# Performance work log

Hardware: AMD Instinct MI355X
Metric: run time of the kernel (lower is better)

The kernel has to match this reference:

```python
import jax, jax.numpy as jnp
import numpy as np

EMBED_DIM = 2048
N_HEADS = 16
N_KV_HEADS = 4
HEAD_DIM = EMBED_DIM // N_HEADS  # 128
B, T = 8, 512


def _rope_tables(seq, dim):
    # matches RoPE.__init__: freqs repeated twice along last dim
    inv_freq = 1.0 / (10000.0 ** (jnp.arange(0, dim, 2, dtype=jnp.float32) / dim))
    t = jnp.arange(seq, dtype=jnp.float32)
    freqs = jnp.outer(t, inv_freq)          # [T, dim/2]
    emb = jnp.concatenate([freqs, freqs], axis=-1)  # [T, dim]
    return jnp.cos(emb), jnp.sin(emb)


def _apply_rope(x, cos, sin):
    # x: [B, H, T, D]; rotate-half convention
    d2 = x.shape[-1] // 2
    x1, x2 = x[..., :d2], x[..., d2:]
    x_rot = jnp.concatenate([-x2, x1], axis=-1)
    return x * cos[None, None] + x_rot * sin[None, None]


def setup_inputs() -> dict:
    key = jax.random.key(0)
    k1, k2, k3, k4, k5 = jax.random.split(key, 5)
    x = jax.random.normal(k1, (B, T, EMBED_DIM), dtype=jnp.float32)
    s = 1.0 / np.sqrt(EMBED_DIM)
    # weights stored [in, out] for y = x @ W
    wq = jax.random.normal(k2, (EMBED_DIM, EMBED_DIM), dtype=jnp.float32) * s
    wk = jax.random.normal(k3, (EMBED_DIM, HEAD_DIM * N_KV_HEADS), dtype=jnp.float32) * s
    wv = jax.random.normal(k4, (EMBED_DIM, HEAD_DIM * N_KV_HEADS), dtype=jnp.float32) * s
    wo = jax.random.normal(k5, (EMBED_DIM, EMBED_DIM), dtype=jnp.float32) * s
    # causal mask: 1 where attendable, 0 -> masked to -inf
    mask = jnp.tril(jnp.ones((T, T), dtype=bool))[None, None]  # [1,1,T,T]
    return {"x": x, "wq": wq, "wk": wk, "wv": wv, "wo": wo, "mask": mask}


def reference(x, wq, wk, wv, wo, mask):
    Bx, Tx, C = x.shape
    rep = N_HEADS // N_KV_HEADS
    q = (x @ wq).reshape(Bx, Tx, N_HEADS, HEAD_DIM).transpose(0, 2, 1, 3)      # [B,H,T,D]
    k = (x @ wk).reshape(Bx, Tx, N_KV_HEADS, HEAD_DIM).transpose(0, 2, 1, 3)   # [B,Hk,T,D]
    v = (x @ wv).reshape(Bx, Tx, N_KV_HEADS, HEAD_DIM).transpose(0, 2, 1, 3)
    cos, sin = _rope_tables(Tx, HEAD_DIM)
    q = _apply_rope(q, cos, sin)
    k = _apply_rope(k, cos, sin)
    k = jnp.repeat(k, rep, axis=1)  # GQA expand -> [B,H,T,D]
    v = jnp.repeat(v, rep, axis=1)
    scale = HEAD_DIM ** -0.5
    attn = jnp.einsum('bhtd,bhsd->bhts', q, k) * scale  # [B,H,T,T]
    attn = jnp.where(mask, attn, -jnp.inf)
    attn = jax.nn.softmax(attn, axis=-1)
    out = jnp.einsum('bhts,bhsd->bhtd', attn, v)        # [B,H,T,D]
    out = out.transpose(0, 2, 1, 3).reshape(Bx, Tx, C)
    return out @ wo
```

## Files before the change

kernel.cpp:

```cpp
#include <hip/hip_runtime.h>
#include <hip/hip_bf16.h>
#include <stdint.h>


typedef __bf16 bf16x8 __attribute__((ext_vector_type(8)));
typedef float  f32x4  __attribute__((ext_vector_type(4)));
typedef float  f4     __attribute__((ext_vector_type(4)));
typedef unsigned short u16x8 __attribute__((ext_vector_type(8)));
typedef unsigned short u16x4 __attribute__((ext_vector_type(4)));
typedef unsigned short us;

template<int V> struct Ic { static constexpr int v = V; };

__device__ __forceinline__ float bf2f(us u) {
  unsigned int x = ((unsigned int)u) << 16;
  return __builtin_bit_cast(float, x);
}
__device__ __forceinline__ us f2bf(float f) {
  unsigned int x = __builtin_bit_cast(unsigned int, f);
  unsigned int r = x + 0x7fffu + ((x >> 16) & 1u);
  return (us)(r >> 16);
}

__device__ __forceinline__ void gload16(const void* gsrc, void* ldst) {
  auto g = (const __attribute__((address_space(1))) void*)gsrc;
  auto l = (__attribute__((address_space(3))) void*)ldst;
  __builtin_amdgcn_global_load_lds(g, l, 16, 0, 0);
}

#define BAR() __builtin_amdgcn_s_barrier()
#define LGK0() do { asm volatile("s_waitcnt lgkmcnt(0)" ::: "memory"); \
                    __builtin_amdgcn_sched_barrier(0); } while (0)

template<int N> __device__ __forceinline__ void VMW() {
  if constexpr (N == 0)      asm volatile("s_waitcnt vmcnt(0)" ::: "memory");
  else if constexpr (N == 2) asm volatile("s_waitcnt vmcnt(2)" ::: "memory");
  else if constexpr (N == 3) asm volatile("s_waitcnt vmcnt(3)" ::: "memory");
  else if constexpr (N == 4) asm volatile("s_waitcnt vmcnt(4)" ::: "memory");
  else static_assert(N == 0 || N == 2 || N == 3 || N == 4, "unsupported vmcnt");
  __builtin_amdgcn_sched_barrier(0);
}


__global__ void convx_kernel(const float* __restrict__ x, us* __restrict__ xb) {
  size_t idx = (size_t)blockIdx.x * 256 + threadIdx.x;
  const f4* p = (const f4*)(x + idx * 8);
  f4 a = p[0], b = p[1];
  u16x8 o;
#pragma unroll
  for (int e = 0; e < 4; ++e) { o[e] = f2bf(a[e]); o[4 + e] = f2bf(b[e]); }
  *(u16x8*)(xb + idx * 8) = o;
}

__global__ __launch_bounds__(256) void wtrans_all_kernel(
    const float* __restrict__ wq, const float* __restrict__ wk,
    const float* __restrict__ wv, const float* __restrict__ wo,
    us* __restrict__ wcat, us* __restrict__ wot) {
  __shared__ float lds[64][65];
  int bx = blockIdx.x;
  const float* src; us* dst; int N, rowOff, nb;
  if (bx < 32)      { src = wq; dst = wcat; N = 2048; rowOff = 0;    nb = bx; }
  else if (bx < 40) { src = wk; dst = wcat; N = 512;  rowOff = 2048; nb = bx - 32; }
  else if (bx < 48) { src = wv; dst = wcat; N = 512;  rowOff = 2560; nb = bx - 40; }
  else              { src = wo; dst = wot;  N = 2048; rowOff = 0;    nb = bx - 48; }
  const int n0 = nb * 64, k0 = blockIdx.y * 64;
  const int c = threadIdx.x & 63, rq = threadIdx.x >> 6;
#pragma unroll
  for (int i = 0; i < 16; ++i) {
    int r = i * 4 + rq;
    lds[r][c] = src[(size_t)(k0 + r) * N + n0 + c];
  }
  __syncthreads();
#pragma unroll
  for (int i = 0; i < 16; ++i) {
    int nr = i * 4 + rq;
    dst[(size_t)(rowOff + n0 + nr) * 2048 + k0 + c] = f2bf(lds[c][nr]);
  }
}

__global__ void tables_kernel(float* __restrict__ ct, float* __restrict__ st) {
  int idx = blockIdx.x * 256 + threadIdx.x;
  int i = idx & 63, t = idx >> 6;
  float inv = exp2f(-(float)i * (13.287712379549449f / 64.0f));
  float ang = (float)t * inv;
  ct[idx] = cosf(ang);
  st[idx] = sinf(ang);
}

__global__ void rope_kernel(us* __restrict__ Qh, us* __restrict__ Kh,
                            const float* __restrict__ ct, const float* __restrict__ st) {
  int idx = blockIdx.x * 256 + threadIdx.x;
  int dq = idx & 15;
  int t = (idx >> 4) & 511;
  int slot = idx >> 13;
  bool isQ = slot < 128;
  us* rowp = isQ ? (Qh + ((size_t)slot * 512 + t) * 128)
                 : (Kh + ((size_t)(slot - 128) * 512 + t) * 128);
  int d0 = dq * 4;
  u16x4 x1 = *(const u16x4*)(rowp + d0);
  u16x4 x2 = *(const u16x4*)(rowp + 64 + d0);
  f4 c = *(const f4*)(ct + t * 64 + d0);
  f4 s = *(const f4*)(st + t * 64 + d0);
  float scale = isQ ? 0.08838834764831845f : 1.0f;
  u16x4 o1, o2;
#pragma unroll
  for (int e = 0; e < 4; ++e) {
    float a = bf2f(x1[e]), b = bf2f(x2[e]);
    o1[e] = f2bf((a * c[e] - b * s[e]) * scale);
    o2[e] = f2bf((b * c[e] + a * s[e]) * scale);
  }
  *(u16x4*)(rowp + d0) = o1;
  *(u16x4*)(rowp + 64 + d0) = o2;
}

__global__ __launch_bounds__(256) void vtrans_kernel(const us* __restrict__ Vh,
                                                     us* __restrict__ Vt) {
  __shared__ us lds[64][66];
  const int bid = blockIdx.x;
  const int bhk = bid >> 4;
  const int rem = bid & 15;
  const int tt = rem >> 1, dt = rem & 1;
  const us* src = Vh + (size_t)bhk * 512 * 128;
  us* dst = Vt + (size_t)bhk * 128 * 512;
  const int c = threadIdx.x & 63, rq = threadIdx.x >> 6;
#pragma unroll
  for (int i = 0; i < 16; ++i) {
    int r = i * 4 + rq;
    lds[r][c] = src[(size_t)(tt * 64 + r) * 128 + dt * 64 + c];
  }
  __syncthreads();
#pragma unroll
  for (int i = 0; i < 16; ++i) {
    int dr = i * 4 + rq;
    dst[(size_t)(dt * 64 + dr) * 512 + tt * 64 + c] = lds[c][dr];
  }
}

template<int BM, int BN, int WM, int WN>
__device__ __forceinline__ void gemm8_core(const us* __restrict__ A,
    const us* __restrict__ Bt, const int K, const int m0, const int n0,
    us* sm, f32x4 (&acc)[BM / (16 * WM)][BN / (16 * WN)]) {
  constexpr int MF = BM / (16 * WM), NF = BN / (16 * WN);
  constexpr int MH = MF / 2, NH = NF / 2;
  constexpr int QM = MH * 16, QN = NH * 16;
  constexpr int AHALF = (BM / 2) * 64, ABUF = BM * 64, ALDS = 2 * ABUF;
  constexpr int BHALF = (BN / 2) * 64, BBUF = BN * 64;
  constexpr int AL = BM / 128, BL = BN / 128;
  const int tid = threadIdx.x, lane = tid & 63, wid = tid >> 6;
  const int wm = wid / WN, wn = wid % WN;
  const int lr = lane & 15, lq = lane >> 4;

  const f32x4 zz = {0.f, 0.f, 0.f, 0.f};
#pragma unroll
  for (int i = 0; i < MF; ++i)
#pragma unroll
    for (int j = 0; j < NF; ++j) acc[i][j] = zz;

  bf16x8 afr[MH][2], bfr[NH][2];

  auto stageA = [&](int kt, int qd, int h) {
#pragma unroll
    for (int i = 0; i < AL; ++i) {
      int c = i * 512 + tid;
      int lrow = c >> 3;
      int grow = (lrow / QM) * (2 * QM) + h * QM + (lrow % QM);
      int kcs = (c & 7) ^ (lrow & 7);
      gload16(A + (size_t)(m0 + grow) * K + (kt << 6) + (kcs << 3),
              sm + qd * ABUF + h * AHALF + c * 8);
    }
  };
  auto stageB = [&](int kt, int qd, int h) {
#pragma unroll
    for (int i = 0; i < BL; ++i) {
      int c = i * 512 + tid;
      int lrow = c >> 3;
      int grow = (lrow / QN) * (2 * QN) + h * QN + (lrow % QN);
      int kcs = (c & 7) ^ (lrow & 7);
      gload16(Bt + (size_t)(n0 + grow) * K + (kt << 6) + (kcs << 3),
              sm + ALDS + qd * BBUF + h * BHALF + c * 8);
    }
  };
  auto lda = [&](int q, int h) {
#pragma unroll
    for (int f = 0; f < MH; ++f) {
      int R = wm * QM + f * 16 + lr;
      const char* base = (const char*)(sm + q * ABUF + h * AHALF + R * 64);
      int sw = (R & 7) << 4;
#pragma unroll
      for (int ks = 0; ks < 2; ++ks)
        afr[f][ks] = *(const bf16x8*)(base + ((ks * 64 + lq * 16) ^ sw));
    }
  };
  auto ldb = [&](int q, int h) {
#pragma unroll
    for (int g = 0; g < NH; ++g) {
      int R = wn * QN + g * 16 + lr;
      const char* base = (const char*)(sm + ALDS + q * BBUF + h * BHALF + R * 64);
      int sw = (R & 7) << 4;
#pragma unroll
      for (int ks = 0; ks < 2; ++ks)
        bfr[g][ks] = *(const bf16x8*)(base + ((ks * 64 + lq * 16) ^ sw));
    }
  };
  auto mmac = [&](auto MQ, auto NQ) {
    constexpr int mq = decltype(MQ)::v, nq = decltype(NQ)::v;
    __builtin_amdgcn_s_setprio(1);
#pragma unroll
    for (int ks = 0; ks < 2; ++ks)
#pragma unroll
      for (int f = 0; f < MH; ++f)
#pragma unroll
        for (int g = 0; g < NH; ++g)
          acc[mq * MH + f][nq * NH + g] = __builtin_amdgcn_mfma_f32_16x16x32_bf16(
              afr[f][ks], bfr[g][ks], acc[mq * MH + f][nq * NH + g], 0, 0, 0);
    __builtin_amdgcn_s_setprio(0);
  };

  stageA(0, 0, 0); stageB(0, 0, 0); stageB(0, 0, 1); stageA(0, 0, 1);
  VMW<AL + BL>(); BAR();

  const int NT = K >> 6;
  for (int kt = 0; kt < NT; ++kt) {
    const int q = kt & 1, qn = q ^ 1;
    const bool pf = (kt + 1 < NT);
    lda(q, 0); ldb(q, 0);
    if (pf) stageA(kt + 1, qn, 0);
    BAR(); LGK0(); mmac(Ic<0>{}, Ic<0>{});
    if (pf) VMW<2 * AL>(); else VMW<AL>();
    BAR();
    ldb(q, 1);
    if (pf) stageB(kt + 1, qn, 0);
    BAR(); LGK0(); mmac(Ic<0>{}, Ic<1>{});
    if (pf) VMW<AL + BL>(); else VMW<0>();
    BAR();
    lda(q, 1);
    if (pf) stageB(kt + 1, qn, 1);
    BAR(); LGK0(); mmac(Ic<1>{}, Ic<1>{});
    BAR();
    ldb(q, 0);
    if (pf) stageA(kt + 1, qn, 1);
    BAR(); LGK0(); mmac(Ic<1>{}, Ic<0>{});
    if (pf) VMW<AL + BL>();
    BAR();
  }
}

__global__ __launch_bounds__(512, 2) void gemm_qkv8_kernel(const us* __restrict__ xb,
    const us* __restrict__ wcat, us* __restrict__ Qh, us* __restrict__ Kh,
    us* __restrict__ Vh) {
  __shared__ __align__(16) us sm[65536];
  const int bid = blockIdx.x;
  const int swz = (bid & 7) * 24 + (bid >> 3);
  const int m0 = (swz & 15) << 8, n0 = (swz >> 4) << 8;
  f32x4 acc[8][4];
  gemm8_core<256, 256, 2, 4>(xb, wcat, 2048, m0, n0, sm, acc);

  const int tid = threadIdx.x, lane = tid & 63, wid = tid >> 6;
  const int wm = wid >> 2, wn = wid & 3, lr = lane & 15, lq = lane >> 4;
#pragma unroll
  for (int f = 0; f < 8; ++f)
#pragma unroll
    for (int g = 0; g < 4; ++g) {
      int col = n0 + wn * 64 + g * 16 + lr;
#pragma unroll
      for (int r = 0; r < 4; ++r) {
        int row = m0 + wm * 128 + f * 16 + lq * 4 + r;
        int bb = row >> 9, t = row & 511;
        us val = f2bf(acc[f][g][r]);
        if (col < 2048) {
          Qh[((size_t)(bb * 16 + (col >> 7)) * 512 + t) * 128 + (col & 127)] = val;
        } else if (col < 2560) {
          int cc = col - 2048;
          Kh[((size_t)(bb * 4 + (cc >> 7)) * 512 + t) * 128 + (cc & 127)] = val;
        } else {
          int cc = col - 2560;
          Vh[((size_t)(bb * 4 + (cc >> 7)) * 512 + t) * 128 + (cc & 127)] = val;
        }
      }
    }
}

__global__ __launch_bounds__(512, 2) void gemm_out8_kernel(const us* __restrict__ Ob,
    const us* __restrict__ wot, float* __restrict__ out) {
  __shared__ __align__(16) us sm[49152];
  const int bid = blockIdx.x;
  const int swz = (bid & 7) * 32 + (bid >> 3);
  const int m0 = (swz & 15) << 8, n0 = (swz >> 4) << 7;
  f32x4 acc[8][2];
  gemm8_core<256, 128, 2, 4>(Ob, wot, 2048, m0, n0, sm, acc);

  const int tid = threadIdx.x, lane = tid & 63, wid = tid >> 6;
  const int wm = wid >> 2, wn = wid & 3, lr = lane & 15, lq = lane >> 4;
#pragma unroll
  for (int f = 0; f < 8; ++f)
#pragma unroll
    for (int g = 0; g < 2; ++g) {
      int col = n0 + wn * 32 + g * 16 + lr;
#pragma unroll
      for (int r = 0; r < 4; ++r) {
        int row = m0 + wm * 128 + f * 16 + lq * 4 + r;
        out[(size_t)row * 2048 + col] = acc[f][g][r];
      }
    }
}

__global__ __launch_bounds__(256) void attn_kernel(const us* __restrict__ Qh,
    const us* __restrict__ Kh, const us* __restrict__ Vt, us* __restrict__ Oh) {
  __shared__ __align__(16) us Ktile[64 * 128];
  __shared__ __align__(16) us Vtile[128 * 64];
  __shared__ __align__(16) us Plds[4 * 16 * 72];
  const int tid = threadIdx.x, lane = tid & 63, w = tid >> 6;
  const int lr = lane & 15, lq = lane >> 4;
  const int qb = blockIdx.x, bh = blockIdx.y;
  const int b = bh >> 4, h = bh & 15, kvh = h >> 2;
  const us* Kbh = Kh + (size_t)(b * 4 + kvh) * 512 * 128;
  const us* Vbh = Vt + (size_t)(b * 4 + kvh) * 128 * 512;

  const us* Qrow = Qh + ((size_t)bh * 512 + qb * 64 + w * 16 + lr) * 128;
  bf16x8 qf[4];
#pragma unroll
  for (int ks = 0; ks < 4; ++ks) qf[ks] = *(const bf16x8*)(Qrow + ks * 32 + (lq << 3));

  const f32x4 zz = {0.f, 0.f, 0.f, 0.f};
  f32x4 o[8];
#pragma unroll
  for (int i = 0; i < 8; ++i) o[i] = zz;
  float m[4], ll[4];
#pragma unroll
  for (int r = 0; r < 4; ++r) { m[r] = -1e30f; ll[r] = 0.f; }
  us* Pw = Plds + w * 16 * 72;

  for (int j = 0; j <= qb; ++j) {
    __syncthreads();
#pragma unroll
    for (int it = 0; it < 4; ++it) {
      int c = it * 256 + tid;
      int row = c >> 4, kc = c & 15;
      gload16(Kbh + (size_t)(j * 64 + row) * 128 + ((kc ^ (row & 7)) << 3),
              Ktile + (c << 3));
    }
#pragma unroll
    for (int it = 0; it < 4; ++it) {
      int c = it * 256 + tid;
      int row = c >> 3, tc = c & 7;
      gload16(Vbh + (size_t)row * 512 + j * 64 + ((tc ^ (row & 7)) << 3),
              Vtile + (c << 3));
    }
    __syncthreads();

    f32x4 s[4];
#pragma unroll
    for (int nb = 0; nb < 4; ++nb) s[nb] = zz;
#pragma unroll
    for (int ks = 0; ks < 4; ++ks) {
#pragma unroll
      for (int nb = 0; nb < 4; ++nb) {
        int row = nb * 16 + lr;
        bf16x8 kf = *(const bf16x8*)(Ktile + (row << 7) + (((ks * 4 + lq) ^ (row & 7)) << 3));
        s[nb] = __builtin_amdgcn_mfma_f32_16x16x32_bf16(qf[ks], kf, s[nb], 0, 0, 0);
      }
    }
    if (j == qb) {
#pragma unroll
      for (int nb = 0; nb < 4; ++nb)
#pragma unroll
        for (int r = 0; r < 4; ++r)
          if (nb * 16 + lr > w * 16 + lq * 4 + r) s[nb][r] = -1e30f;
    }

    float tm[4], alpha[4], rs[4];
#pragma unroll
    for (int r = 0; r < 4; ++r)
      tm[r] = fmaxf(fmaxf(s[0][r], s[1][r]), fmaxf(s[2][r], s[3][r]));
#pragma unroll
    for (int off = 1; off < 16; off <<= 1)
#pragma unroll
      for (int r = 0; r < 4; ++r)
        tm[r] = fmaxf(tm[r], __shfl_xor(tm[r], off, 64));
#pragma unroll
    for (int r = 0; r < 4; ++r) {
      float mn = fmaxf(m[r], tm[r]);
      alpha[r] = __expf(m[r] - mn);
      m[r] = mn;
    }
#pragma unroll
    for (int nb = 0; nb < 4; ++nb)
#pragma unroll
      for (int r = 0; r < 4; ++r)
        s[nb][r] = __expf(s[nb][r] - m[r]);
#pragma unroll
    for (int r = 0; r < 4; ++r)
      rs[r] = s[0][r] + s[1][r] + s[2][r] + s[3][r];
#pragma unroll
    for (int off = 1; off < 16; off <<= 1)
#pragma unroll
      for (int r = 0; r < 4; ++r)
        rs[r] += __shfl_xor(rs[r], off, 64);
#pragma unroll
    for (int r = 0; r < 4; ++r) ll[r] = ll[r] * alpha[r] + rs[r];
#pragma unroll
    for (int i = 0; i < 8; ++i)
#pragma unroll
      for (int r = 0; r < 4; ++r) o[i][r] *= alpha[r];

#pragma unroll
    for (int nb = 0; nb < 4; ++nb)
#pragma unroll
      for (int r = 0; r < 4; ++r)
        Pw[(lq * 4 + r) * 72 + nb * 16 + lr] = f2bf(s[nb][r]);

#pragma unroll
    for (int ks2 = 0; ks2 < 2; ++ks2) {
      bf16x8 pf = *(const bf16x8*)(Pw + lr * 72 + ks2 * 32 + (lq << 3));
#pragma unroll
      for (int nd = 0; nd < 8; ++nd) {
        int d = nd * 16 + lr;
        bf16x8 vf = *(const bf16x8*)(Vtile + (d << 6) + (((ks2 * 4 + lq) ^ (d & 7)) << 3));
        o[nd] = __builtin_amdgcn_mfma_f32_16x16x32_bf16(pf, vf, o[nd], 0, 0, 0);
      }
    }
  }

  float inv[4];
#pragma unroll
  for (int r = 0; r < 4; ++r) inv[r] = 1.0f / ll[r];
  const int rowb = b * 512 + qb * 64 + w * 16 + lq * 4;
  const int colb = h * 128 + lr;
#pragma unroll
  for (int nd = 0; nd < 8; ++nd)
#pragma unroll
    for (int r = 0; r < 4; ++r)
      Oh[(size_t)(rowb + r) * 2048 + colb + nd * 16] = f2bf(o[nd][r] * inv[r]);
}

extern "C" void kernel_launch(void* const* d_in, const int* in_sizes, int n_in,
                              void* d_out, int out_size, void* d_ws, size_t ws_size,
                              hipStream_t stream) {
  const float* x  = (const float*)d_in[0];
  const float* wq = (const float*)d_in[1];
  const float* wk = (const float*)d_in[2];
  const float* wv = (const float*)d_in[3];
  const float* wo = (const float*)d_in[4];
  float* out = (float*)d_out;
  char* ws = (char*)d_ws;

  us*    xb   = (us*)(ws);
  us*    wcat = (us*)(ws + 16777216);
  us*    wot  = (us*)(ws + 29360128);
  us*    Qh   = (us*)(ws + 37748736);
  us*    Kh   = (us*)(ws + 54525952);
  us*    Vh   = (us*)(ws + 58720256);
  us*    Vt   = (us*)(ws + 62914560);
  us*    Oh   = (us*)(ws + 67108864);
  float* ct   = (float*)(ws + 83886080);
  float* st   = (float*)(ws + 84017152);

  convx_kernel<<<4096, 256, 0, stream>>>(x, xb);
  wtrans_all_kernel<<<dim3(80, 32), 256, 0, stream>>>(wq, wk, wv, wo, wcat, wot);
  tables_kernel<<<128, 256, 0, stream>>>(ct, st);

  gemm_qkv8_kernel<<<192, 512, 0, stream>>>(xb, wcat, Qh, Kh, Vh);
  rope_kernel<<<5120, 256, 0, stream>>>(Qh, Kh, ct, st);
  vtrans_kernel<<<512, 256, 0, stream>>>(Vh, Vt);
  attn_kernel<<<dim3(8, 128), 256, 0, stream>>>(Qh, Kh, Vt, Oh);
  gemm_out8_kernel<<<256, 512, 0, stream>>>(Oh, wot, out);
}
```

Measured before the change: 175.0 us.

## Fuse prep kernels, apply Q RoPE in attention, write V transposed from QKV GEMM

Merges the x conversion, weight transposes and RoPE-table kernels into one prep launch. Replaces the pipelined 256x256 QKV GEMM with a simpler 128x128 single-buffered GEMM that writes V directly in transposed layout, which removes the separate V-transpose kernel. Q RoPE and scaling move into the attention kernel's Q load, so only K gets a standalone RoPE pass. Launch count and intermediate traffic drop, but the new GEMM has no software pipelining and scatters strided 2-byte stores for V.

```diff
diff --git a/kernel.cpp b/kernel.cpp
--- a/kernel.cpp
+++ b/kernel.cpp
@@ -41,99 +41,164 @@
   __builtin_amdgcn_sched_barrier(0);
 }
 
-
-__global__ void convx_kernel(const float* __restrict__ x, us* __restrict__ xb) {
-  size_t idx = (size_t)blockIdx.x * 256 + threadIdx.x;
-  const f4* p = (const f4*)(x + idx * 8);
-  f4 a = p[0], b = p[1];
-  u16x8 o;
-#pragma unroll
-  for (int e = 0; e < 4; ++e) { o[e] = f2bf(a[e]); o[4 + e] = f2bf(b[e]); }
-  *(u16x8*)(xb + idx * 8) = o;
-}
-
-__global__ __launch_bounds__(256) void wtrans_all_kernel(
-    const float* __restrict__ wq, const float* __restrict__ wk,
-    const float* __restrict__ wv, const float* __restrict__ wo,
-    us* __restrict__ wcat, us* __restrict__ wot) {
-  __shared__ float lds[64][65];
-  int bx = blockIdx.x;
-  const float* src; us* dst; int N, rowOff, nb;
-  if (bx < 32)      { src = wq; dst = wcat; N = 2048; rowOff = 0;    nb = bx; }
-  else if (bx < 40) { src = wk; dst = wcat; N = 512;  rowOff = 2048; nb = bx - 32; }
-  else if (bx < 48) { src = wv; dst = wcat; N = 512;  rowOff = 2560; nb = bx - 40; }
-  else              { src = wo; dst = wot;  N = 2048; rowOff = 0;    nb = bx - 48; }
-  const int n0 = nb * 64, k0 = blockIdx.y * 64;
-  const int c = threadIdx.x & 63, rq = threadIdx.x >> 6;
-#pragma unroll
-  for (int i = 0; i < 16; ++i) {
-    int r = i * 4 + rq;
-    lds[r][c] = src[(size_t)(k0 + r) * N + n0 + c];
+__global__ __launch_bounds__(256) void prep_kernel(
+    const float* __restrict__ x, const float* __restrict__ wq,
+    const float* __restrict__ wk, const float* __restrict__ wv,
+    const float* __restrict__ wo, us* __restrict__ xb,
+    us* __restrict__ wcat, us* __restrict__ wot,
+    float* __restrict__ ct, float* __restrict__ st) {
+  const int bid = blockIdx.x, tid = threadIdx.x;
+  if (bid < 4096) {
+    size_t idx = (size_t)bid * 256 + tid;
+    const f4* p = (const f4*)(x + idx * 8);
+    f4 a = p[0], b = p[1];
+    u16x8 o;
+#pragma unroll
+    for (int e = 0; e < 4; ++e) { o[e] = f2bf(a[e]); o[4 + e] = f2bf(b[e]); }
+    *(u16x8*)(xb + idx * 8) = o;
+  } else if (bid < 6656) {
+    __shared__ float lds[64][65];
+    int lb = bid - 4096;
+    int bx = lb % 80, ky = lb / 80;
+    const float* src; us* dst; int N, rowOff, nb;
+    if (bx < 32)      { src = wq; dst = wcat; N = 2048; rowOff = 0;    nb = bx; }
+    else if (bx < 40) { src = wk; dst = wcat; N = 512;  rowOff = 2048; nb = bx - 32; }
+    else if (bx < 48) { src = wv; dst = wcat; N = 512;  rowOff = 2560; nb = bx - 40; }
+    else              { src = wo; dst = wot;  N = 2048; rowOff = 0;    nb = bx - 48; }
+    const int n0 = nb * 64, k0 = ky * 64;
+    const int c = tid & 63, rq = tid >> 6;
+#pragma unroll
+    for (int i = 0; i < 16; ++i) {
+      int r = i * 4 + rq;
+      lds[r][c] = src[(size_t)(k0 + r) * N + n0 + c];
+    }
+    __syncthreads();
+#pragma unroll
+    for (int i = 0; i < 16; ++i) {
+      int nr = i * 4 + rq;
+      dst[(size_t)(rowOff + n0 + nr) * 2048 + k0 + c] = f2bf(lds[c][nr]);
+    }
+  } else {
+    int idx = (bid - 6656) * 256 + tid;
+    int i = idx & 63, t = idx >> 6;
+    float inv = exp2f(-(float)i * (13.287712379549449f / 64.0f));
+    float ang = (float)t * inv;
+    ct[idx] = cosf(ang);
+    st[idx] = sinf(ang);
   }
-  __syncthreads();
-#pragma unroll
-  for (int i = 0; i < 16; ++i) {
-    int nr = i * 4 + rq;
-    dst[(size_t)(rowOff + n0 + nr) * 2048 + k0 + c] = f2bf(lds[c][nr]);
-  }
-}
-
-__global__ void tables_kernel(float* __restrict__ ct, float* __restrict__ st) {
-  int idx = blockIdx.x * 256 + threadIdx.x;
-  int i = idx & 63, t = idx >> 6;
-  float inv = exp2f(-(float)i * (13.287712379549449f / 64.0f));
-  float ang = (float)t * inv;
-  ct[idx] = cosf(ang);
-  st[idx] = sinf(ang);
-}
-
-__global__ void rope_kernel(us* __restrict__ Qh, us* __restrict__ Kh,
-                            const float* __restrict__ ct, const float* __restrict__ st) {
+}
+
+__global__ void rope_k_kernel(us* __restrict__ Kh,
+                              const float* __restrict__ ct, const float* __restrict__ st) {
   int idx = blockIdx.x * 256 + threadIdx.x;
   int dq = idx & 15;
   int t = (idx >> 4) & 511;
   int slot = idx >> 13;
-  bool isQ = slot < 128;
-  us* rowp = isQ ? (Qh + ((size_t)slot * 512 + t) * 128)
-                 : (Kh + ((size_t)(slot - 128) * 512 + t) * 128);
+  us* rowp = Kh + ((size_t)slot * 512 + t) * 128;
   int d0 = dq * 4;
   u16x4 x1 = *(const u16x4*)(rowp + d0);
   u16x4 x2 = *(const u16x4*)(rowp + 64 + d0);
   f4 c = *(const f4*)(ct + t * 64 + d0);
   f4 s = *(const f4*)(st + t * 64 + d0);
-  float scale = isQ ? 0.08838834764831845f : 1.0f;
   u16x4 o1, o2;
 #pragma unroll
   for (int e = 0; e < 4; ++e) {
     float a = bf2f(x1[e]), b = bf2f(x2[e]);
-    o1[e] = f2bf((a * c[e] - b * s[e]) * scale);
-    o2[e] = f2bf((b * c[e] + a * s[e]) * scale);
+    o1[e] = f2bf(a * c[e] - b * s[e]);
+    o2[e] = f2bf(b * c[e] + a * s[e]);
   }
   *(u16x4*)(rowp + d0) = o1;
   *(u16x4*)(rowp + 64 + d0) = o2;
 }
 
-__global__ __launch_bounds__(256) void vtrans_kernel(const us* __restrict__ Vh,
-                                                     us* __restrict__ Vt) {
-  __shared__ us lds[64][66];
+__device__ __forceinline__ void gemm2_core(const us* __restrict__ A,
+    const us* __restrict__ Bt, const int K, const int m0, const int n0,
+    us* AT, us* BT, f32x4 (&acc)[4][4]) {
+  const int tid = threadIdx.x;
+  const int lane = tid & 63;
+  const int wid = tid >> 6;
+  const int wm = wid >> 1, wn = wid & 1;
+  const int lr = lane & 15, lq = lane >> 4;
+  const f32x4 zz = {0.f, 0.f, 0.f, 0.f};
+#pragma unroll
+  for (int i = 0; i < 4; ++i)
+#pragma unroll
+    for (int j = 0; j < 4; ++j) acc[i][j] = zz;
+
+  const int KT = K >> 6;
+  for (int kt = 0; kt < KT; ++kt) {
+    __syncthreads();
+#pragma unroll
+    for (int i = 0; i < 4; ++i) {
+      int c = i * 256 + tid;
+      int row = c >> 3, kc = (c & 7) ^ (row & 7);
+      gload16(A + (size_t)(m0 + row) * K + (kt << 6) + (kc << 3), AT + c * 8);
+    }
+#pragma unroll
+    for (int i = 0; i < 4; ++i) {
+      int c = i * 256 + tid;
+      int row = c >> 3, kc = (c & 7) ^ (row & 7);
+      gload16(Bt + (size_t)(n0 + row) * K + (kt << 6) + (kc << 3), BT + c * 8);
+    }
+    __syncthreads();
+#pragma unroll
+    for (int ks = 0; ks < 2; ++ks) {
+      bf16x8 af[4], bfm[4];
+#pragma unroll
+      for (int i = 0; i < 4; ++i) {
+        int R = wm * 64 + i * 16 + lr;
+        af[i] = *(const bf16x8*)((const char*)AT + R * 128 +
+                                 ((ks * 64 + lq * 16) ^ ((R & 7) << 4)));
+      }
+#pragma unroll
+      for (int j = 0; j < 4; ++j) {
+        int R = wn * 64 + j * 16 + lr;
+        bfm[j] = *(const bf16x8*)((const char*)BT + R * 128 +
+                                  ((ks * 64 + lq * 16) ^ ((R & 7) << 4)));
+      }
+#pragma unroll
+      for (int i = 0; i < 4; ++i)
+#pragma unroll
+        for (int j = 0; j < 4; ++j)
+          acc[i][j] = __builtin_amdgcn_mfma_f32_16x16x32_bf16(af[i], bfm[j], acc[i][j], 0, 0, 0);
+    }
+  }
+}
+
+__global__ __launch_bounds__(256, 4) void gemm_qkv2_kernel(const us* __restrict__ xb,
+    const us* __restrict__ wcat, us* __restrict__ Qh, us* __restrict__ Kh,
+    us* __restrict__ Vt) {
+  __shared__ __align__(16) us AT[128 * 64];
+  __shared__ __align__(16) us BT[128 * 64];
   const int bid = blockIdx.x;
-  const int bhk = bid >> 4;
-  const int rem = bid & 15;
-  const int tt = rem >> 1, dt = rem & 1;
-  const us* src = Vh + (size_t)bhk * 512 * 128;
-  us* dst = Vt + (size_t)bhk * 128 * 512;
-  const int c = threadIdx.x & 63, rq = threadIdx.x >> 6;
-#pragma unroll
-  for (int i = 0; i < 16; ++i) {
-    int r = i * 4 + rq;
-    lds[r][c] = src[(size_t)(tt * 64 + r) * 128 + dt * 64 + c];
-  }
-  __syncthreads();
-#pragma unroll
-  for (int i = 0; i < 16; ++i) {
-    int dr = i * 4 + rq;
-    dst[(size_t)(dt * 64 + dr) * 512 + tt * 64 + c] = lds[c][dr];
-  }
+  const int swz = (bid & 7) * 96 + (bid >> 3);
+  const int m0 = (swz & 31) << 7, n0 = (swz >> 5) << 7;
+  f32x4 acc[4][4];
+  gemm2_core(xb, wcat, 2048, m0, n0, AT, BT, acc);
+
+  const int tid = threadIdx.x, lane = tid & 63, wid = tid >> 6;
+  const int wm = wid >> 1, wn = wid & 1, lr = lane & 15, lq = lane >> 4;
+#pragma unroll
+  for (int i = 0; i < 4; ++i)
+#pragma unroll
+    for (int j = 0; j < 4; ++j) {
+      int col = n0 + wn * 64 + j * 16 + lr;
+#pragma unroll
+      for (int r = 0; r < 4; ++r) {
+        int row = m0 + wm * 64 + i * 16 + lq * 4 + r;
+        int bb = row >> 9, t = row & 511;
+        us val = f2bf(acc[i][j][r]);
+        if (col < 2048) {
+          Qh[((size_t)(bb * 16 + (col >> 7)) * 512 + t) * 128 + (col & 127)] = val;
+        } else if (col < 2560) {
+          int cc = col - 2048;
+          Kh[((size_t)(bb * 4 + (cc >> 7)) * 512 + t) * 128 + (cc & 127)] = val;
+        } else {
+          int cc = col - 2560;
+          Vt[((size_t)(bb * 4 + (cc >> 7)) * 128 + (cc & 127)) * 512 + t] = val;
+        }
+      }
+    }
 }
 
 template<int BM, int BN, int WM, int WN>
@@ -245,41 +310,6 @@
   }
 }
 
-__global__ __launch_bounds__(512, 2) void gemm_qkv8_kernel(const us* __restrict__ xb,
-    const us* __restrict__ wcat, us* __restrict__ Qh, us* __restrict__ Kh,
-    us* __restrict__ Vh) {
-  __shared__ __align__(16) us sm[65536];
-  const int bid = blockIdx.x;
-  const int swz = (bid & 7) * 24 + (bid >> 3);
-  const int m0 = (swz & 15) << 8, n0 = (swz >> 4) << 8;
-  f32x4 acc[8][4];
-  gemm8_core<256, 256, 2, 4>(xb, wcat, 2048, m0, n0, sm, acc);
-
-  const int tid = threadIdx.x, lane = tid & 63, wid = tid >> 6;
-  const int wm = wid >> 2, wn = wid & 3, lr = lane & 15, lq = lane >> 4;
-#pragma unroll
-  for (int f = 0; f < 8; ++f)
-#pragma unroll
-    for (int g = 0; g < 4; ++g) {
-      int col = n0 + wn * 64 + g * 16 + lr;
-#pragma unroll
-      for (int r = 0; r < 4; ++r) {
-        int row = m0 + wm * 128 + f * 16 + lq * 4 + r;
-        int bb = row >> 9, t = row & 511;
-        us val = f2bf(acc[f][g][r]);
-        if (col < 2048) {
-          Qh[((size_t)(bb * 16 + (col >> 7)) * 512 + t) * 128 + (col & 127)] = val;
-        } else if (col < 2560) {
-          int cc = col - 2048;
-          Kh[((size_t)(bb * 4 + (cc >> 7)) * 512 + t) * 128 + (cc & 127)] = val;
-        } else {
-          int cc = col - 2560;
-          Vh[((size_t)(bb * 4 + (cc >> 7)) * 512 + t) * 128 + (cc & 127)] = val;
-        }
-      }
-    }
-}
-
 __global__ __launch_bounds__(512, 2) void gemm_out8_kernel(const us* __restrict__ Ob,
     const us* __restrict__ wot, float* __restrict__ out) {
   __shared__ __align__(16) us sm[49152];
@@ -305,7 +335,8 @@
 }
 
 __global__ __launch_bounds__(256) void attn_kernel(const us* __restrict__ Qh,
-    const us* __restrict__ Kh, const us* __restrict__ Vt, us* __restrict__ Oh) {
+    const us* __restrict__ Kh, const us* __restrict__ Vt, us* __restrict__ Oh,
+    const float* __restrict__ ct, const float* __restrict__ st) {
   __shared__ __align__(16) us Ktile[64 * 128];
   __shared__ __align__(16) us Vtile[128 * 64];
   __shared__ __align__(16) us Plds[4 * 16 * 72];
@@ -316,10 +347,28 @@
   const us* Kbh = Kh + (size_t)(b * 4 + kvh) * 512 * 128;
   const us* Vbh = Vt + (size_t)(b * 4 + kvh) * 128 * 512;
 
-  const us* Qrow = Qh + ((size_t)bh * 512 + qb * 64 + w * 16 + lr) * 128;
+  const int t_abs = qb * 64 + w * 16 + lr;
+  const us* Qrow = Qh + ((size_t)bh * 512 + t_abs) * 128;
   bf16x8 qf[4];
-#pragma unroll
-  for (int ks = 0; ks < 4; ++ks) qf[ks] = *(const bf16x8*)(Qrow + ks * 32 + (lq << 3));
+  {
+    const float* cp = ct + t_abs * 64 + (lq << 3);
+    const float* sp = st + t_abs * 64 + (lq << 3);
+#pragma unroll
+    for (int ks = 0; ks < 2; ++ks) {
+      u16x8 a = *(const u16x8*)(Qrow + ks * 32 + (lq << 3));
+      u16x8 bb2 = *(const u16x8*)(Qrow + 64 + ks * 32 + (lq << 3));
+      u16x8 oa, ob;
+#pragma unroll
+      for (int e = 0; e < 8; ++e) {
+        float c = cp[ks * 32 + e], s = sp[ks * 32 + e];
+        float av = bf2f(a[e]), bv = bf2f(bb2[e]);
+        oa[e] = f2bf((av * c - bv * s) * 0.08838834764831845f);
+        ob[e] = f2bf((bv * c + av * s) * 0.08838834764831845f);
+      }
+      qf[ks] = __builtin_bit_cast(bf16x8, oa);
+      qf[ks + 2] = __builtin_bit_cast(bf16x8, ob);
+    }
+  }
 
   const f32x4 zz = {0.f, 0.f, 0.f, 0.f};
   f32x4 o[8];
@@ -449,19 +498,14 @@
   us*    wot  = (us*)(ws + 29360128);
   us*    Qh   = (us*)(ws + 37748736);
   us*    Kh   = (us*)(ws + 54525952);
-  us*    Vh   = (us*)(ws + 58720256);
-  us*    Vt   = (us*)(ws + 62914560);
+  us*    Vt   = (us*)(ws + 58720256);
   us*    Oh   = (us*)(ws + 67108864);
   float* ct   = (float*)(ws + 83886080);
   float* st   = (float*)(ws + 84017152);
 
-  convx_kernel<<<4096, 256, 0, stream>>>(x, xb);
-  wtrans_all_kernel<<<dim3(80, 32), 256, 0, stream>>>(wq, wk, wv, wo, wcat, wot);
-  tables_kernel<<<128, 256, 0, stream>>>(ct, st);
-
-  gemm_qkv8_kernel<<<192, 512, 0, stream>>>(xb, wcat, Qh, Kh, Vh);
-  rope_kernel<<<5120, 256, 0, stream>>>(Qh, Kh, ct, st);
-  vtrans_kernel<<<512, 256, 0, stream>>>(Vh, Vt);
-  attn_kernel<<<dim3(8, 128), 256, 0, stream>>>(Qh, Kh, Vt, Oh);
+  prep_kernel<<<6784, 256, 0, stream>>>(x, wq, wk, wv, wo, xb, wcat, wot, ct, st);
+  gemm_qkv2_kernel<<<768, 256, 0, stream>>>(xb, wcat, Qh, Kh, Vt);
+  rope_k_kernel<<<1024, 256, 0, stream>>>(Kh, ct, st);
+  attn_kernel<<<dim3(8, 128), 256, 0, stream>>>(Qh, Kh, Vt, Oh, ct, st);
   gemm_out8_kernel<<<256, 512, 0, stream>>>(Oh, wot, out);
 }
```

Measured after the change: 176.9 us. No clear change (+1.1%).
